# Kernel optimization log

Measured on AMD Instinct MI355X. Metric: run time of the kernel, lower is better.

Reference implementation:

```python
import jax, jax.numpy as jnp
import numpy as np

# Original torch code does the CZT in float64/complex128 explicitly; match it.
jax.config.update("jax_enable_x64", True)

SR = 44100
HOP = 512
MAX_NHAR = 128
REL_WIN = 4
F0_MIN = 40.0  # reconstruction of get_n_fft(): lowest analyzable pitch
N_MAX = int(round(SR / F0_MIN * REL_WIN / 2) * 2)          # 4410: max window size
N_FFT = int(2 ** np.ceil(np.log2(N_MAX)))                  # 8192: used only for padding
L = int(2 ** np.ceil(np.log2(N_MAX + MAX_NHAR - 1)))       # 8192: Bluestein conv length (exact for all frames since L >= n_i + m_i - 1)
N_FRAMES = 1024


def setup_inputs() -> dict:
    key = jax.random.key(0)
    k1, k2 = jax.random.split(key)
    t = N_FRAMES * HOP
    x = jax.random.normal(k1, (t,), dtype=jnp.float32)
    # pitch contour in a realistic 100..400 Hz voice range
    f0 = 100.0 + 300.0 * jax.random.uniform(k2, (N_FRAMES,), dtype=jnp.float32)
    return {"x": x, "f0": f0}


def _sinusoidal_analysis_czt(x, f0):
    # f0: (F,). Vectorized, padded/masked version of the per-frame CZT loop.
    f0 = jnp.clip(f0.astype(jnp.float64), F0_MIN, None)
    F = f0.shape[0]
    nhar = jnp.minimum(jnp.floor(SR / f0 / 2.0), float(MAX_NHAR)).astype(jnp.int32)      # (F,)
    winsize = (jnp.round(SR / f0 * REL_WIN / 2.0) * 2).astype(jnp.int32)                 # (F,) even, <= N_MAX
    pad = N_FFT // 2
    x_pad = jnp.pad(x.astype(jnp.float64), (pad, pad))

    j = jnp.arange(N_MAX)
    start = jnp.arange(F) * HOP + pad                                                    # (F,)
    idx = start[:, None] - winsize[:, None] // 2 + j[None, :]                            # (F, N_MAX)
    frames = x_pad[jnp.clip(idx, 0, x_pad.shape[0] - 1)]
    # torch.blackman_window(n) is periodic: denominator = n
    ratio = j[None, :].astype(jnp.float64) / winsize[:, None].astype(jnp.float64)
    win = 0.42 - 0.5 * jnp.cos(2.0 * np.pi * ratio) + 0.08 * jnp.cos(4.0 * np.pi * ratio)
    valid = j[None, :] < winsize[:, None]
    xw = jnp.where(valid, frames * win, 0.0)                                             # (F, N_MAX) windowed frame, zero-padded

    theta = 2.0 * np.pi * f0 / SR                                                        # (F,) A=exp(+i th), W=exp(-i th)
    jj = j.astype(jnp.float64)
    # gn[j] = x[j] * A^{-j} * W^{j^2/2} = x[j] * exp(-i th (j + j^2/2))
    gphase = -theta[:, None] * (jj[None, :] + 0.5 * jj[None, :] ** 2)
    gn = jnp.zeros((F, L), dtype=jnp.complex128).at[:, :N_MAX].set(xw * jnp.exp(1j * gphase))
    # hn[k] = 1/w[k] = exp(+i th k^2/2) for k < m ; hn[L-j] = exp(+i th j^2/2) for 1 <= j < n
    # (filled for the max ranges; extra entries are never reached because gn is zero beyond winsize)
    kk = jnp.arange(L)
    off = jnp.where(kk < MAX_NHAR, kk, jnp.where(kk > L - N_MAX, L - kk, 0)).astype(jnp.float64)
    hmask = (kk < MAX_NHAR) | (kk > L - N_MAX)
    hn = jnp.where(hmask[None, :], jnp.exp(1j * theta[:, None] * 0.5 * off[None, :] ** 2), 0.0 + 0.0j)
    qn = jnp.fft.ifft(jnp.fft.fft(gn, axis=-1) * jnp.fft.fft(hn, axis=-1), axis=-1)      # (F, L)

    m = jnp.arange(MAX_NHAR).astype(jnp.float64)
    wq = jnp.exp(-1j * theta[:, None] * 0.5 * m[None, :] ** 2)                           # w[:m]
    yn = qn[:, :MAX_NHAR] * wq                                                           # (F, MAX_NHAR)
    yn = 2.381 * yn / (winsize[:, None] // 2 + 1).astype(jnp.float64)
    har_mask = m[None, :] < nhar[:, None].astype(jnp.float64)
    ampl = jnp.where(har_mask, jnp.abs(yn), 0.0).T.astype(jnp.float32)                   # (MAX_NHAR, F)
    phase = jnp.where(har_mask, jnp.angle(yn), 0.0).T.astype(jnp.float32)
    return ampl, phase


def reference(x, f0):
    return _sinusoidal_analysis_czt(x, f0)
```

## Files before the change

### kernel.cpp

```cpp
#include <hip/hip_runtime.h>

#define HOP 512
#define MAX_NHAR 128
#define N_MAX 4410
#define CHUNK_MAX 1104
#define PI_D 3.14159265358979323846

__device__ __forceinline__ void frame_params(double f0v, int& w, int& nhar, double& theta) {
    double f0d = f0v < 40.0 ? 40.0 : f0v;
    const double inv = 44100.0 / f0d;
    nhar = (int)fmin(floor(inv * 0.5), 128.0);
    w = 2 * (int)rint(inv * 2.0);
    if (w > N_MAX) w = N_MAX;
    theta = (2.0 * PI_D * f0d) / 44100.0;
}

__device__ __forceinline__ int chunk_of(int w, int segs) {
    return (((w + segs - 1) / segs) + 3) & ~3;
}

__global__ __launch_bounds__(128) void prep_kernel(
    const float* __restrict__ f0, double* __restrict__ ccos, int F)
{
    const int f = blockIdx.x, k = threadIdx.x;
    int w, nhar; double theta;
    frame_params((double)f0[f], w, nhar, theta);
    ccos[f * MAX_NHAR + k] = cos(theta * (double)(k + 1));
}

template <int SEGS>
__global__ __launch_bounds__(128) void goertzel_kernel(
    const float* __restrict__ x, const float* __restrict__ f0,
    const double* __restrict__ ccos, double2* __restrict__ parts,
    int t, int F)
{
    __shared__ double sm[CHUNK_MAX];
    const int frame = blockIdx.x / SEGS;
    const int seg   = blockIdx.x % SEGS;
    const int tid   = threadIdx.x;

    int w, nhar; double theta;
    frame_params((double)f0[frame], w, nhar, theta);

    const int chunk = chunk_of(w, SEGS);
    const int j0 = seg * chunk;
    int len = w - j0; if (len > chunk) len = chunk; if (len < 0) len = 0;

    {
        const double c2pi_invw = (2.0 * PI_D) / (double)w;
        const int base = frame * HOP - (w >> 1) + j0;
        for (int j = tid; j < len; j += 128) {
            const int ix = base + j;
            const double val = (ix >= 0 && ix < t) ? (double)x[ix] : 0.0;
            const double c1 = cos(c2pi_invw * (double)(j0 + j));
            const double win = fma(0.16, c1 * c1, 0.34) - 0.5 * c1;
            sm[j] = val * win;
        }
    }
    __syncthreads();

    const int kbase = tid & ~63;
    const int mylen = (kbase >= nhar) ? 0 : len;
    const double C = 2.0 * ccos[frame * MAX_NHAR + tid];
    double s1 = 0.0, s2 = 0.0;
    #pragma unroll 4
    for (int j = 0; j < mylen; ++j) {
        const double s0 = fma(C, s1, sm[j] - s2);
        s2 = s1; s1 = s0;
    }
    parts[(size_t)(frame * SEGS + seg) * MAX_NHAR + tid] = make_double2(s1, s2);
}

template <int SEGS>
__global__ __launch_bounds__(128) void finalize_kernel(
    const float* __restrict__ f0, const double2* __restrict__ parts,
    float* __restrict__ out, int F)
{
    const int frame = blockIdx.x;
    const int tid = threadIdx.x;

    int w, nhar; double theta;
    frame_params((double)f0[frame], w, nhar, theta);
    const int chunk = chunk_of(w, SEGS);
    const double omega = theta * (double)(tid + 1);

    double sw, cw; sincos(omega, &sw, &cw);
    double sq, cq; sincos(omega * (double)chunk, &sq, &cq);
    double sl, cl; sincos(omega * (double)(w - 1), &sl, &cl);

    double Rr = cq * cw + sq * sw, Ri = cq * sw - sq * cw;
    double yr = 0.0, yi = 0.0;
    const double2* p = parts + (size_t)frame * SEGS * MAX_NHAR + tid;
    #pragma unroll
    for (int s = 0; s < SEGS; ++s) {
        const double2 v = p[(size_t)s * MAX_NHAR];
        const double tr = fma(-cw, v.y, v.x);
        const double ti = sw * v.y;
        const double Pr = (s == SEGS - 1) ? cl : Rr;
        const double Pi = (s == SEGS - 1) ? -sl : Ri;
        yr = fma(Pr, tr, fma(-Pi, ti, yr));
        yi = fma(Pr, ti, fma( Pi, tr, yi));
        const double nr = Rr * cq + Ri * sq;
        Ri = Ri * cq - Rr * sq; Rr = nr;
    }
    const double scale = 2.381 / (double)((w >> 1) + 1);
    yr *= scale; yi *= scale;

    float ampl = 0.0f, ph = 0.0f;
    if (tid < nhar) {
        ampl = (float)sqrt(yr * yr + yi * yi);
        ph   = (float)atan2(yi, yr);
    }
    out[tid * F + frame] = ampl;
    out[MAX_NHAR * F + tid * F + frame] = ph;
}

__global__ __launch_bounds__(128) void czt_direct_kernel(
    const float* __restrict__ x, const float* __restrict__ f0,
    float* __restrict__ out, int t, int F)
{
    __shared__ double sm[N_MAX];
    const int frame = blockIdx.x;
    const int tid = threadIdx.x;
    int w, nhar; double theta;
    frame_params((double)f0[frame], w, nhar, theta);
    {
        const double invw = 1.0 / (double)w;
        double sa, ca, ss, cs;
        sincos((2.0 * PI_D) * ((double)tid * invw), &sa, &ca);
        sincos((2.0 * PI_D) * (128.0 * invw), &ss, &cs);
        double zr = ca, zi = sa;
        const int base = frame * HOP - (w >> 1);
        for (int j = tid; j < w; j += 128) {
            const int ix = base + j;
            const double val = (ix >= 0 && ix < t) ? (double)x[ix] : 0.0;
            const double c = zr;
            const double win = 0.42 - 0.5 * c + 0.08 * (2.0 * c * c - 1.0);
            sm[j] = val * win;
            const double nzr = zr * cs - zi * ss;
            zi = zr * ss + zi * cs;
            zr = nzr;
        }
    }
    __syncthreads();
    double s, c;
    sincos(theta * (double)(tid + 1), &s, &c);
    const double rr = c, ri = -s;
    const double r2r = rr * rr - ri * ri, r2i = 2.0 * rr * ri;
    const double r4r = r2r * r2r - r2i * r2i, r4i = 2.0 * r2r * r2i;
    const double r3r = r2r * rr - r2i * ri, r3i = r2r * ri + r2i * rr;
    double z0r = 1.0, z0i = 0.0, z1r = rr, z1i = ri;
    double z2r = r2r, z2i = r2i, z3r = r3r, z3i = r3i;
    double a0r = 0, a0i = 0, a1r = 0, a1i = 0, a2r = 0, a2i = 0, a3r = 0, a3i = 0;
    const int w4 = w & ~3;
    for (int j = 0; j < w4; j += 4) {
        const double s0 = sm[j], s1 = sm[j + 1], s2 = sm[j + 2], s3 = sm[j + 3];
        double tr;
        a0r = fma(s0, z0r, a0r); a0i = fma(s0, z0i, a0i);
        tr = z0r * r4r - z0i * r4i; z0i = z0r * r4i + z0i * r4r; z0r = tr;
        a1r = fma(s1, z1r, a1r); a1i = fma(s1, z1i, a1i);
        tr = z1r * r4r - z1i * r4i; z1i = z1r * r4i + z1i * r4r; z1r = tr;
        a2r = fma(s2, z2r, a2r); a2i = fma(s2, z2i, a2i);
        tr = z2r * r4r - z2i * r4i; z2i = z2r * r4i + z2i * r4r; z2r = tr;
        a3r = fma(s3, z3r, a3r); a3i = fma(s3, z3i, a3i);
        tr = z3r * r4r - z3i * r4i; z3i = z3r * r4i + z3i * r4r; z3r = tr;
    }
    if (w4 < w) {
        const double s0 = sm[w4], s1 = sm[w4 + 1];
        a0r = fma(s0, z0r, a0r); a0i = fma(s0, z0i, a0i);
        a1r = fma(s1, z1r, a1r); a1i = fma(s1, z1i, a1i);
    }
    double yr = (a0r + a1r) + (a2r + a3r);
    double yi = (a0i + a1i) + (a2i + a3i);
    const double scale = 2.381 / (double)((w >> 1) + 1);
    yr *= scale; yi *= scale;
    float ampl = 0.0f, ph = 0.0f;
    if (tid < nhar) {
        ampl = (float)sqrt(yr * yr + yi * yi);
        ph   = (float)atan2(yi, yr);
    }
    out[tid * F + frame] = ampl;
    out[MAX_NHAR * F + tid * F + frame] = ph;
}

extern "C" void kernel_launch(void* const* d_in, const int* in_sizes, int n_in,
                              void* d_out, int out_size, void* d_ws, size_t ws_size,
                              hipStream_t stream) {
    const float* x  = (const float*)d_in[0];
    const float* f0 = (const float*)d_in[1];
    float* out = (float*)d_out;
    const int t = in_sizes[0];
    const int F = in_sizes[1];

    const size_t table_bytes = (size_t)F * MAX_NHAR * sizeof(double);
    const size_t need8 = table_bytes + (size_t)F * 8 * MAX_NHAR * sizeof(double2);
    const size_t need4 = table_bytes + (size_t)F * 4 * MAX_NHAR * sizeof(double2);

    if (ws_size >= need8) {
        double* ccos = (double*)d_ws;
        double2* parts = (double2*)((char*)d_ws + table_bytes);
        prep_kernel<<<F, 128, 0, stream>>>(f0, ccos, F);
        goertzel_kernel<8><<<F * 8, 128, 0, stream>>>(x, f0, ccos, parts, t, F);
        finalize_kernel<8><<<F, 128, 0, stream>>>(f0, parts, out, F);
    } else if (ws_size >= need4) {
        double* ccos = (double*)d_ws;
        double2* parts = (double2*)((char*)d_ws + table_bytes);
        prep_kernel<<<F, 128, 0, stream>>>(f0, ccos, F);
        goertzel_kernel<4><<<F * 4, 128, 0, stream>>>(x, f0, ccos, parts, t, F);
        finalize_kernel<4><<<F, 128, 0, stream>>>(f0, parts, out, F);
    } else {
        czt_direct_kernel<<<F, 128, 0, stream>>>(x, f0, out, t, F);
    }
}
```

Baseline: 82.65 us.

## Precompute windowed frames globally and run two harmonics per lane in Goertzel

```diff
diff --git a/kernel.cpp b/kernel.cpp
--- a/kernel.cpp
+++ b/kernel.cpp
@@ -3,7 +3,8 @@
 #define HOP 512
 #define MAX_NHAR 128
 #define N_MAX 4410
-#define CHUNK_MAX 1104
+#define ROWP 4416
+#define SEGS 8
 #define PI_D 3.14159265358979323846
 
 __device__ __forceinline__ void frame_params(double f0v, int& w, int& nhar, double& theta) {
@@ -15,63 +16,98 @@
     theta = (2.0 * PI_D * f0d) / 44100.0;
 }
 
-__device__ __forceinline__ int chunk_of(int w, int segs) {
-    return (((w + segs - 1) / segs) + 3) & ~3;
+__device__ __forceinline__ int chunk8_of(int w) {
+    return (((w + SEGS - 1) / SEGS) + 7) & ~7;
 }
 
 __global__ __launch_bounds__(128) void prep_kernel(
-    const float* __restrict__ f0, double* __restrict__ ccos, int F)
-{
-    const int f = blockIdx.x, k = threadIdx.x;
+    const float* __restrict__ x, const float* __restrict__ f0,
+    double* __restrict__ ccos, double* __restrict__ xw, int t, int F)
+{
+    const int f = blockIdx.x, tid = threadIdx.x;
     int w, nhar; double theta;
     frame_params((double)f0[f], w, nhar, theta);
-    ccos[f * MAX_NHAR + k] = cos(theta * (double)(k + 1));
-}
-
-template <int SEGS>
-__global__ __launch_bounds__(128) void goertzel_kernel(
-    const float* __restrict__ x, const float* __restrict__ f0,
-    const double* __restrict__ ccos, double2* __restrict__ parts,
-    int t, int F)
-{
-    __shared__ double sm[CHUNK_MAX];
-    const int frame = blockIdx.x / SEGS;
-    const int seg   = blockIdx.x % SEGS;
-    const int tid   = threadIdx.x;
-
-    int w, nhar; double theta;
-    frame_params((double)f0[frame], w, nhar, theta);
-
-    const int chunk = chunk_of(w, SEGS);
-    const int j0 = seg * chunk;
-    int len = w - j0; if (len > chunk) len = chunk; if (len < 0) len = 0;
-
-    {
-        const double c2pi_invw = (2.0 * PI_D) / (double)w;
-        const int base = frame * HOP - (w >> 1) + j0;
-        for (int j = tid; j < len; j += 128) {
+    ccos[f * MAX_NHAR + tid] = cos(theta * (double)(tid + 1));
+
+    const double invw = 1.0 / (double)w;
+    double sa, ca, ss, cs;
+    sincos((2.0 * PI_D) * ((double)tid * invw), &sa, &ca);
+    sincos((2.0 * PI_D) * (128.0 * invw), &ss, &cs);
+    double zr = ca, zi = sa;
+    const int base = f * HOP - (w >> 1);
+    double* row = xw + (size_t)f * ROWP;
+    for (int j = tid; j < ROWP; j += 128) {
+        double outv = 0.0;
+        if (j < w) {
             const int ix = base + j;
             const double val = (ix >= 0 && ix < t) ? (double)x[ix] : 0.0;
-            const double c1 = cos(c2pi_invw * (double)(j0 + j));
-            const double win = fma(0.16, c1 * c1, 0.34) - 0.5 * c1;
-            sm[j] = val * win;
-        }
-    }
-    __syncthreads();
-
-    const int kbase = tid & ~63;
-    const int mylen = (kbase >= nhar) ? 0 : len;
-    const double C = 2.0 * ccos[frame * MAX_NHAR + tid];
-    double s1 = 0.0, s2 = 0.0;
-    #pragma unroll 4
-    for (int j = 0; j < mylen; ++j) {
-        const double s0 = fma(C, s1, sm[j] - s2);
-        s2 = s1; s1 = s0;
-    }
-    parts[(size_t)(frame * SEGS + seg) * MAX_NHAR + tid] = make_double2(s1, s2);
-}
-
-template <int SEGS>
+            const double c = zr;
+            const double win = 0.42 - 0.5 * c + 0.08 * (2.0 * c * c - 1.0);
+            outv = val * win;
+        }
+        row[j] = outv;
+        const double nzr = zr * cs - zi * ss;
+        zi = zr * ss + zi * cs;
+        zr = nzr;
+    }
+}
+
+__global__ __launch_bounds__(64) void goertzel_kernel(
+    const float* __restrict__ f0, const double* __restrict__ ccos,
+    const double* __restrict__ xw, double2* __restrict__ parts, int F)
+{
+    const int frame = blockIdx.x >> 3;
+    const int seg   = blockIdx.x & (SEGS - 1);
+    const int lane  = threadIdx.x;
+
+    int w, nhar; double theta;
+    frame_params((double)f0[frame], w, nhar, theta);
+    const int chunk = chunk8_of(w);
+    const int j0 = seg * chunk;
+    int lenp = 0;
+    if (j0 < w) {
+        const int l = w - j0;
+        lenp = (l > chunk) ? chunk : ((l + 7) & ~7);
+    }
+
+    const double Ca = 2.0 * ccos[frame * MAX_NHAR + lane];
+    const double Cb = 2.0 * ccos[frame * MAX_NHAR + lane + 64];
+    double s1a = 0.0, s2a = 0.0, s1b = 0.0, s2b = 0.0;
+    const double* __restrict__ row = xw + (size_t)frame * ROWP + j0;
+
+    if (nhar > 64) {
+        for (int jb = 0; jb < lenp; jb += 8) {
+            double xv[8];
+            #pragma unroll
+            for (int u = 0; u < 8; ++u) xv[u] = row[jb + u];
+            #pragma unroll
+            for (int u = 0; u < 8; ++u) {
+                const double ta = xv[u] - s2a;
+                const double tb = xv[u] - s2b;
+                const double na = fma(Ca, s1a, ta);
+                const double nb = fma(Cb, s1b, tb);
+                s2a = s1a; s1a = na;
+                s2b = s1b; s1b = nb;
+            }
+        }
+    } else {
+        for (int jb = 0; jb < lenp; jb += 8) {
+            double xv[8];
+            #pragma unroll
+            for (int u = 0; u < 8; ++u) xv[u] = row[jb + u];
+            #pragma unroll
+            for (int u = 0; u < 8; ++u) {
+                const double ta = xv[u] - s2a;
+                const double na = fma(Ca, s1a, ta);
+                s2a = s1a; s1a = na;
+            }
+        }
+    }
+    double2* p = parts + (size_t)(frame * SEGS + seg) * MAX_NHAR;
+    p[lane]      = make_double2(s1a, s2a);
+    p[lane + 64] = make_double2(s1b, s2b);
+}
+
 __global__ __launch_bounds__(128) void finalize_kernel(
     const float* __restrict__ f0, const double2* __restrict__ parts,
     float* __restrict__ out, int F)
@@ -81,12 +117,14 @@
 
     int w, nhar; double theta;
     frame_params((double)f0[frame], w, nhar, theta);
-    const int chunk = chunk_of(w, SEGS);
+    const int chunk = chunk8_of(w);
+    const int slast = (w - 1) / chunk;
+    const int endlast = slast * chunk + (((w - slast * chunk) + 7) & ~7);
     const double omega = theta * (double)(tid + 1);
 
     double sw, cw; sincos(omega, &sw, &cw);
     double sq, cq; sincos(omega * (double)chunk, &sq, &cq);
-    double sl, cl; sincos(omega * (double)(w - 1), &sl, &cl);
+    double sl, cl; sincos(omega * (double)(endlast - 1), &sl, &cl);
 
     double Rr = cq * cw + sq * sw, Ri = cq * sw - sq * cw;
     double yr = 0.0, yi = 0.0;
@@ -96,8 +134,8 @@
         const double2 v = p[(size_t)s * MAX_NHAR];
         const double tr = fma(-cw, v.y, v.x);
         const double ti = sw * v.y;
-        const double Pr = (s == SEGS - 1) ? cl : Rr;
-        const double Pi = (s == SEGS - 1) ? -sl : Ri;
+        const double Pr = (s == slast) ? cl : Rr;
+        const double Pi = (s == slast) ? -sl : Ri;
         yr = fma(Pr, tr, fma(-Pi, ti, yr));
         yi = fma(Pr, ti, fma( Pi, tr, yi));
         const double nr = Rr * cq + Ri * sq;
@@ -192,22 +230,16 @@
     const int t = in_sizes[0];
     const int F = in_sizes[1];
 
-    const size_t table_bytes = (size_t)F * MAX_NHAR * sizeof(double);
-    const size_t need8 = table_bytes + (size_t)F * 8 * MAX_NHAR * sizeof(double2);
-    const size_t need4 = table_bytes + (size_t)F * 4 * MAX_NHAR * sizeof(double2);
-
-    if (ws_size >= need8) {
-        double* ccos = (double*)d_ws;
-        double2* parts = (double2*)((char*)d_ws + table_bytes);
-        prep_kernel<<<F, 128, 0, stream>>>(f0, ccos, F);
-        goertzel_kernel<8><<<F * 8, 128, 0, stream>>>(x, f0, ccos, parts, t, F);
-        finalize_kernel<8><<<F, 128, 0, stream>>>(f0, parts, out, F);
-    } else if (ws_size >= need4) {
-        double* ccos = (double*)d_ws;
-        double2* parts = (double2*)((char*)d_ws + table_bytes);
-        prep_kernel<<<F, 128, 0, stream>>>(f0, ccos, F);
-        goertzel_kernel<4><<<F * 4, 128, 0, stream>>>(x, f0, ccos, parts, t, F);
-        finalize_kernel<4><<<F, 128, 0, stream>>>(f0, parts, out, F);
+    const size_t ccos_b  = (size_t)F * MAX_NHAR * sizeof(double);
+    const size_t xw_b    = (size_t)F * ROWP * sizeof(double);
+    const size_t parts_b = (size_t)F * SEGS * MAX_NHAR * sizeof(double2);
+    if (ws_size >= ccos_b + xw_b + parts_b) {
+        double*  ccos  = (double*)d_ws;
+        double*  xw    = (double*)((char*)d_ws + ccos_b);
+        double2* parts = (double2*)((char*)d_ws + ccos_b + xw_b);
+        prep_kernel<<<F, 128, 0, stream>>>(x, f0, ccos, xw, t, F);
+        goertzel_kernel<<<F * SEGS, 64, 0, stream>>>(f0, ccos, xw, parts, F);
+        finalize_kernel<<<F, 128, 0, stream>>>(f0, parts, out, F);
     } else {
         czt_direct_kernel<<<F, 128, 0, stream>>>(x, f0, out, t, F);
     }
```

Result: slower. 92.04 us (+11.4%).
